# Kernel optimization log

Hardware: AMD Instinct MI355X
Metric: run time of the kernel (lower is better)

The kernel has to match this reference:

```python
import jax, jax.numpy as jnp
import numpy as np

N, C, T, V = 64, 64, 256, 25
REL, OUT = 8, 64
ALPHA = 1.0


def setup_inputs() -> dict:
    key = jax.random.key(0)
    ks = jax.random.split(key, 10)
    s = lambda k, shape: jax.random.normal(k, shape, dtype=jnp.float32) * 0.05
    return {
        "x": jax.random.normal(ks[0], (N, C, T, V), dtype=jnp.float32),
        "A": jax.random.normal(ks[1], (V, V), dtype=jnp.float32),
        "w1": s(ks[2], (REL, C)), "b1": s(ks[3], (REL,)),
        "w2": s(ks[4], (REL, C)), "b2": s(ks[5], (REL,)),
        "w3": s(ks[6], (OUT, C)), "b3": s(ks[7], (OUT,)),
        "w4": s(ks[8], (OUT, REL)), "b4": s(ks[9], (OUT,)),
    }


def reference(x, A, w1, b1, w2, b2, w3, b3, w4, b4):
    # 1x1 conv commutes with the temporal mean, so reduce T first (same math).
    xm = jnp.mean(x, axis=2)                                   # [N, C, V]
    x1 = jnp.einsum('ncv,rc->nrv', xm, w1) + b1[:, None]        # [N, R, V]
    x2 = jnp.einsum('ncv,rc->nrv', xm, w2) + b2[:, None]        # [N, R, V]
    x3 = jnp.einsum('nctv,oc->notv', x, w3) + b3[:, None, None] # [N, O, T, V]
    # dynamic topology: tanh of broadcast difference -> [N, R, V, V]
    adj = jnp.tanh(x1[:, :, :, None] - x2[:, :, None, :])
    # conv4 (1x1 over VxV) then scale + static adjacency
    d = jnp.einsum('nruv,or->nouv', adj, w4) + b4[:, None, None]
    d = d * ALPHA + A[None, None]                               # [N, O, V, V]
    # graph aggregation: out[n,o,t,v] = sum_u d[n,o,u,v] * x3[n,o,t,u]
    return jnp.einsum('nouv,notu->notv', d, x3)
```

## Files before the change

### kernel.cpp

```cpp
#include <hip/hip_runtime.h>

#define N_ 64
#define C_ 64
#define T_ 256
#define V_ 25
#define R_ 8
#define O_ 64
constexpr int TV = T_ * V_;
constexpr float INV_T = 1.0f / (float)T_;
constexpr int TC = 16;
constexpr int NPOS = TC * V_;
constexpr int NT = NPOS / 16;
constexpr int DP = 32;
constexpr int UPAD = 40;
constexpr int X3S = 16 * UPAD + 8;

typedef __attribute__((ext_vector_type(8))) short s8v;
typedef __attribute__((ext_vector_type(4))) short s4v;
typedef __attribute__((ext_vector_type(4))) float f4v;

__device__ __forceinline__ unsigned short f2bf(float f) {
    union { float f; unsigned u; } v; v.f = f;
    unsigned r = v.u + 0x7FFFu + ((v.u >> 16) & 1u);
    return (unsigned short)(r >> 16);
}

__global__ __launch_bounds__(256) void k_mean(const float* __restrict__ x,
                                              float* __restrict__ xm) {
    __shared__ float part[8 * V_];
    const int bid = blockIdx.x;
    const int tid = threadIdx.x;
    const float* xp = x + (size_t)bid * TV;
    if (tid < 200) {
        const int vid = tid % V_;
        const int seg = tid / V_;
        float s = 0.f;
        const float* p = xp + seg * 32 * V_ + vid;
        #pragma unroll
        for (int j = 0; j < 32; ++j) s += p[j * V_];
        part[tid] = s;
    }
    __syncthreads();
    if (tid < V_) {
        float s = 0.f;
        #pragma unroll
        for (int k = 0; k < 8; ++k) s += part[k * V_ + tid];
        xm[(size_t)bid * V_ + tid] = s * INV_T;
    }
}

__global__ __launch_bounds__(256) void k_dmat(const float* __restrict__ xm,
                                              const float* __restrict__ A,
                                              const float* __restrict__ w1,
                                              const float* __restrict__ b1,
                                              const float* __restrict__ w2,
                                              const float* __restrict__ b2,
                                              const float* __restrict__ w4,
                                              const float* __restrict__ b4,
                                              unsigned short* __restrict__ dT) {
    __shared__ float xms[C_][V_];
    __shared__ float x1s[R_][V_];
    __shared__ float x2s[R_][V_];
    const int n  = blockIdx.x;
    const int og = blockIdx.y * 8;
    const int tid = threadIdx.x;

    for (int i = tid; i < C_ * V_; i += 256)
        xms[i / V_][i % V_] = xm[(size_t)n * C_ * V_ + i];
    __syncthreads();

    for (int i = tid; i < 2 * R_ * V_; i += 256) {
        const int j = i % (R_ * V_);
        const int r = j / V_, v = j % V_;
        const bool first = (i < R_ * V_);
        const float* w = first ? w1 : w2;
        float acc = first ? b1[r] : b2[r];
        #pragma unroll
        for (int c = 0; c < C_; ++c) acc += w[r * C_ + c] * xms[c][v];
        if (first) x1s[r][v] = acc;
        else       x2s[r][v] = acc;
    }
    __syncthreads();

    unsigned short* dn = dT + (size_t)n * O_ * DP * DP;
    for (int p = tid; p < DP * DP; p += 256) {
        const int v = p >> 5, u = p & 31;
        if (u < V_ && v < V_) {
            float adjr[R_];
            #pragma unroll
            for (int r = 0; r < R_; ++r) adjr[r] = tanhf(x1s[r][u] - x2s[r][v]);
            const float a = A[u * V_ + v];
            #pragma unroll
            for (int oo = 0; oo < 8; ++oo) {
                const int o = og + oo;
                float acc = b4[o];
                #pragma unroll
                for (int r = 0; r < R_; ++r) acc = fmaf(w4[o * R_ + r], adjr[r], acc);
                dn[(size_t)o * DP * DP + p] = f2bf(acc + a);
            }
        } else {
            #pragma unroll
            for (int oo = 0; oo < 8; ++oo)
                dn[(size_t)(og + oo) * DP * DP + p] = 0;
        }
    }
}

__global__ __launch_bounds__(512, 4) void k_F(const float* __restrict__ x,
                                              const float* __restrict__ w3,
                                              const float* __restrict__ b3,
                                              const unsigned short* __restrict__ dT,
                                              float* __restrict__ out) {
    __shared__ __align__(16) unsigned short xs[NT * 1024];
    __shared__ __align__(16) unsigned short x3b[16 * X3S];

    const int n    = blockIdx.y;
    const int tc   = blockIdx.x;
    const int tid  = threadIdx.x;
    const int lane = tid & 63;
    const int wave = tid >> 6;
    const int l16  = lane & 15;
    const int lg   = lane >> 4;

    if (tid < 256) {
        const int o_l = tid >> 4, t = tid & 15;
        *(s8v*)&x3b[o_l * X3S + t * UPAD + 24] = (s8v)0;
    }

    {
        const float* xb = x + (size_t)n * C_ * TV + tc * NPOS;
        #pragma unroll 1
        for (int i = 0; i < 13; ++i) {
            const int s = i * 512 + tid;
            if (s < 6400) {
                const int c = s / 100, p4 = s - c * 100;
                const float4 v4 = *(const float4*)(xb + (size_t)c * TV + p4 * 4);
                const int pos = p4 * 4;
                const int pt = pos >> 4;
                s4v pk;
                pk[0] = (short)f2bf(v4.x); pk[1] = (short)f2bf(v4.y);
                pk[2] = (short)f2bf(v4.z); pk[3] = (short)f2bf(v4.w);
                *(s4v*)&xs[pt * 1024 + ((c ^ (pt & 7)) << 4) + (pos & 15)] = pk;
            }
        }
    }
    __syncthreads();

    s8v bfr[4][2];
    int ts[4], us[4];
    #pragma unroll
    for (int i = 0; i < 4; ++i) {
        const int nt = wave + 8 * i;
        if (nt < NT) {
            const int pos = nt * 16 + l16;
            ts[i] = pos / 25; us[i] = pos - 25 * ts[i];
            const unsigned short* base = &xs[nt * 1024];
            const int sw = nt & 7;
            #pragma unroll
            for (int kh = 0; kh < 2; ++kh) {
                s8v f;
                #pragma unroll
                for (int j = 0; j < 8; ++j) {
                    const int c = kh * 32 + lg * 8 + j;
                    f[j] = (short)base[((c ^ sw) << 4) + l16];
                }
                bfr[i][kh] = f;
            }
        }
    }

    const unsigned short* dn = dT + (size_t)n * O_ * DP * DP;
    float* on = out + (size_t)n * O_ * TV + tc * NPOS;

    #pragma unroll 1
    for (int h = 0; h < 4; ++h) {
        s8v afr[2];
        #pragma unroll
        for (int kh = 0; kh < 2; ++kh) {
            const float* wp = w3 + (h * 16 + l16) * C_ + kh * 32 + lg * 8;
            s8v f;
            #pragma unroll
            for (int j = 0; j < 8; ++j) f[j] = (short)f2bf(wp[j]);
            afr[kh] = f;
        }
        const f4v b3h = *(const f4v*)(b3 + h * 16 + lg * 4);

        #pragma unroll
        for (int i = 0; i < 4; ++i) {
            const int nt = wave + 8 * i;
            if (nt < NT) {
                f4v acc = (f4v)0.f;
                acc = __builtin_amdgcn_mfma_f32_16x16x32_bf16(afr[0], bfr[i][0], acc, 0, 0, 0);
                acc = __builtin_amdgcn_mfma_f32_16x16x32_bf16(afr[1], bfr[i][1], acc, 0, 0, 0);
                #pragma unroll
                for (int r = 0; r < 4; ++r)
                    x3b[(lg * 4 + r) * X3S + ts[i] * UPAD + us[i]] = f2bf(acc[r] + b3h[r]);
            }
        }
        __syncthreads();

        #pragma unroll
        for (int oo = 0; oo < 2; ++oo) {
            const int o_l = wave * 2 + oo;
            const int o_g = h * 16 + o_l;
            const s8v av  = *(const s8v*)&x3b[o_l * X3S + l16 * UPAD + lg * 8];
            const unsigned short* dp = dn + (size_t)o_g * DP * DP;
            const s8v bv0 = *(const s8v*)(dp + l16 * DP + lg * 8);
            const s8v bv1 = *(const s8v*)(dp + (16 + l16) * DP + lg * 8);
            f4v c0 = (f4v)0.f, c1 = (f4v)0.f;
            c0 = __builtin_amdgcn_mfma_f32_16x16x32_bf16(av, bv0, c0, 0, 0, 0);
            c1 = __builtin_amdgcn_mfma_f32_16x16x32_bf16(av, bv1, c1, 0, 0, 0);
            float* ob = on + (size_t)o_g * TV;
            #pragma unroll
            for (int r = 0; r < 4; ++r) {
                const int t = lg * 4 + r;
                ob[t * 25 + l16] = c0[r];
                if (l16 < 9) ob[t * 25 + 16 + l16] = c1[r];
            }
        }
        __syncthreads();
    }
}

extern "C" void kernel_launch(void* const* d_in, const int* in_sizes, int n_in,
                              void* d_out, int out_size, void* d_ws, size_t ws_size,
                              hipStream_t stream) {
    const float* x  = (const float*)d_in[0];
    const float* A  = (const float*)d_in[1];
    const float* w1 = (const float*)d_in[2];
    const float* b1 = (const float*)d_in[3];
    const float* w2 = (const float*)d_in[4];
    const float* b2 = (const float*)d_in[5];
    const float* w3 = (const float*)d_in[6];
    const float* b3 = (const float*)d_in[7];
    const float* w4 = (const float*)d_in[8];
    const float* b4 = (const float*)d_in[9];

    float* out = (float*)d_out;
    float* xm  = (float*)d_ws;
    unsigned short* dTm = (unsigned short*)(xm + (size_t)N_ * C_ * V_);

    k_mean<<<N_ * C_, 256, 0, stream>>>(x, xm);
    k_dmat<<<dim3(N_, 8), 256, 0, stream>>>(xm, A, w1, b1, w2, b2, w4, b4, dTm);
    k_F<<<dim3(T_ / TC, N_), 512, 0, stream>>>(x, w3, b3, dTm, out);
}
```

Before: 88.46 us.

## Drop x LDS staging; load x fragments directly from global per head group

Removes the shared-memory staging buffer for x and the upfront global-to-LDS copy plus barrier. Each wave now reads its bf16 B-fragments for the first 1x1 conv straight from global memory, converting inside the h loop. The input is therefore re-read four times, once per output head group, with strided scalar loads instead of coalesced float4 loads. The change also prefetches the dynamic-adjacency fragments at the top of each h iteration and raises launch bounds to 6 blocks per CU to exploit the smaller LDS footprint.

```diff
diff --git a/kernel.cpp b/kernel.cpp
--- a/kernel.cpp
+++ b/kernel.cpp
@@ -106,12 +106,11 @@
     }
 }
 
-__global__ __launch_bounds__(512, 4) void k_F(const float* __restrict__ x,
+__global__ __launch_bounds__(512, 6) void k_F(const float* __restrict__ x,
                                               const float* __restrict__ w3,
                                               const float* __restrict__ b3,
                                               const unsigned short* __restrict__ dT,
                                               float* __restrict__ out) {
-    __shared__ __align__(16) unsigned short xs[NT * 1024];
     __shared__ __align__(16) unsigned short x3b[16 * X3S];
 
     const int n    = blockIdx.y;
@@ -127,53 +126,19 @@
         *(s8v*)&x3b[o_l * X3S + t * UPAD + 24] = (s8v)0;
     }
 
-    {
-        const float* xb = x + (size_t)n * C_ * TV + tc * NPOS;
-        #pragma unroll 1
-        for (int i = 0; i < 13; ++i) {
-            const int s = i * 512 + tid;
-            if (s < 6400) {
-                const int c = s / 100, p4 = s - c * 100;
-                const float4 v4 = *(const float4*)(xb + (size_t)c * TV + p4 * 4);
-                const int pos = p4 * 4;
-                const int pt = pos >> 4;
-                s4v pk;
-                pk[0] = (short)f2bf(v4.x); pk[1] = (short)f2bf(v4.y);
-                pk[2] = (short)f2bf(v4.z); pk[3] = (short)f2bf(v4.w);
-                *(s4v*)&xs[pt * 1024 + ((c ^ (pt & 7)) << 4) + (pos & 15)] = pk;
-            }
-        }
-    }
-    __syncthreads();
-
-    s8v bfr[4][2];
-    int ts[4], us[4];
-    #pragma unroll
-    for (int i = 0; i < 4; ++i) {
-        const int nt = wave + 8 * i;
-        if (nt < NT) {
-            const int pos = nt * 16 + l16;
-            ts[i] = pos / 25; us[i] = pos - 25 * ts[i];
-            const unsigned short* base = &xs[nt * 1024];
-            const int sw = nt & 7;
-            #pragma unroll
-            for (int kh = 0; kh < 2; ++kh) {
-                s8v f;
-                #pragma unroll
-                for (int j = 0; j < 8; ++j) {
-                    const int c = kh * 32 + lg * 8 + j;
-                    f[j] = (short)base[((c ^ sw) << 4) + l16];
-                }
-                bfr[i][kh] = f;
-            }
-        }
-    }
-
+    const float* xbase = x + (size_t)n * C_ * TV + tc * NPOS;
     const unsigned short* dn = dT + (size_t)n * O_ * DP * DP;
     float* on = out + (size_t)n * O_ * TV + tc * NPOS;
 
     #pragma unroll 1
     for (int h = 0; h < 4; ++h) {
+        const int o_l0 = wave * 2, o_g0 = h * 16 + o_l0;
+        const unsigned short* dp0 = dn + (size_t)o_g0 * DP * DP;
+        const s8v pv00 = *(const s8v*)(dp0 + l16 * DP + lg * 8);
+        const s8v pv01 = *(const s8v*)(dp0 + (16 + l16) * DP + lg * 8);
+        const s8v pv10 = *(const s8v*)(dp0 + DP * DP + l16 * DP + lg * 8);
+        const s8v pv11 = *(const s8v*)(dp0 + DP * DP + (16 + l16) * DP + lg * 8);
+
         s8v afr[2];
         #pragma unroll
         for (int kh = 0; kh < 2; ++kh) {
@@ -189,12 +154,23 @@
         for (int i = 0; i < 4; ++i) {
             const int nt = wave + 8 * i;
             if (nt < NT) {
+                const int pos = nt * 16 + l16;
+                const int t = pos / 25, u = pos - 25 * t;
+                s8v bfr[2];
+                #pragma unroll
+                for (int kh = 0; kh < 2; ++kh) {
+                    s8v f;
+                    #pragma unroll
+                    for (int j = 0; j < 8; ++j)
+                        f[j] = (short)f2bf(xbase[(size_t)(kh * 32 + lg * 8 + j) * TV + pos]);
+                    bfr[kh] = f;
+                }
                 f4v acc = (f4v)0.f;
-                acc = __builtin_amdgcn_mfma_f32_16x16x32_bf16(afr[0], bfr[i][0], acc, 0, 0, 0);
-                acc = __builtin_amdgcn_mfma_f32_16x16x32_bf16(afr[1], bfr[i][1], acc, 0, 0, 0);
+                acc = __builtin_amdgcn_mfma_f32_16x16x32_bf16(afr[0], bfr[0], acc, 0, 0, 0);
+                acc = __builtin_amdgcn_mfma_f32_16x16x32_bf16(afr[1], bfr[1], acc, 0, 0, 0);
                 #pragma unroll
                 for (int r = 0; r < 4; ++r)
-                    x3b[(lg * 4 + r) * X3S + ts[i] * UPAD + us[i]] = f2bf(acc[r] + b3h[r]);
+                    x3b[(lg * 4 + r) * X3S + t * UPAD + u] = f2bf(acc[r] + b3h[r]);
             }
         }
         __syncthreads();
@@ -204,9 +180,8 @@
             const int o_l = wave * 2 + oo;
             const int o_g = h * 16 + o_l;
             const s8v av  = *(const s8v*)&x3b[o_l * X3S + l16 * UPAD + lg * 8];
-            const unsigned short* dp = dn + (size_t)o_g * DP * DP;
-            const s8v bv0 = *(const s8v*)(dp + l16 * DP + lg * 8);
-            const s8v bv1 = *(const s8v*)(dp + (16 + l16) * DP + lg * 8);
+            const s8v bv0 = oo ? pv10 : pv00;
+            const s8v bv1 = oo ? pv11 : pv01;
             f4v c0 = (f4v)0.f, c1 = (f4v)0.f;
             c0 = __builtin_amdgcn_mfma_f32_16x16x32_bf16(av, bv0, c0, 0, 0, 0);
             c1 = __builtin_amdgcn_mfma_f32_16x16x32_bf16(av, bv1, c1, 0, 0, 0);
```

Result: slower. 207.4 us (+134.5%).
